# Kernel optimization log

Hardware: AMD Instinct MI355X
Metric: run time of the kernel (lower is better)

## Reference

```python
import jax, jax.numpy as jnp
import numpy as np


def cayley_batch(data):
    # data: (b, r, r). Q = (I + skew) @ (I - skew)^{-1}  (torch solve with left=False)
    b, rr, _ = data.shape
    skew = 0.5 * (data - data.transpose(0, 2, 1))
    I = jnp.eye(rr, dtype=data.dtype)
    A = I - skew  # always invertible (skew-symmetric)
    B = I + skew
    # Solve X @ A = B  ->  A^T X^T = B^T
    Q = jnp.linalg.solve(A.transpose(0, 2, 1), B.transpose(0, 2, 1)).transpose(0, 2, 1)
    return Q


def blockdiag_butterfly_multiply(x, w1, w2):
    # x: (batch, n); w1: (k, q, p) with k*p == n; w2: (l, s, r) with l*r == k*q
    batch = x.shape[0]
    k, q, p = w1.shape
    l, s, r = w2.shape
    out1 = jnp.einsum('bkp,kqp->bkq', x.reshape(batch, k, p), w1)  # (batch, k, q)
    # flat (k*q) viewed as (r, l), then transposed -> (batch, l, r)
    out1 = out1.reshape(batch, r, l).transpose(0, 2, 1)
    out2 = jnp.einsum('blr,lsr->bls', out1, w2)  # (batch, l, s)
    # permute to (batch, s, l) and flatten -> (batch, s*l)
    return out2.transpose(0, 2, 1).reshape(batch, s * l)


def setup_inputs() -> dict:
    key = jax.random.key(0)
    k1, k2, k3 = jax.random.split(key, 3)
    n, nblocks = 4096, 64
    bs = n // nblocks  # 64
    x = jax.random.normal(k1, (16384, n), dtype=jnp.float32)
    L = jax.random.normal(k2, (nblocks, bs, bs), dtype=jnp.float32)
    R = jax.random.normal(k3, (nblocks, bs, bs), dtype=jnp.float32)
    return {"x": x, "L": L, "R": R}


def reference(x, L, R):
    # GSOrthogonal.forward with orthogonal=True, method='cayley':
    # orthogonalize L and R, then butterfly multiply with (x, R_orth, L_orth)
    Lq = cayley_batch(L)
    Rq = cayley_batch(R)
    return blockdiag_butterfly_multiply(x, Rq, Lq)
```

## Files before the change

kernel.cpp:

```cpp
#include <hip/hip_runtime.h>
#include <hip/hip_bf16.h>

typedef __bf16 bf16x4 __attribute__((ext_vector_type(4)));
typedef __bf16 bf16x8 __attribute__((ext_vector_type(8)));
typedef float  floatx4 __attribute__((ext_vector_type(4)));

__global__ __launch_bounds__(256) void cayley_pack_kernel(
    const float* __restrict__ L, const float* __restrict__ R,
    __bf16* __restrict__ ws) {
  __shared__ float Ms[64][65];
  __shared__ float Pa[2][64];
  __shared__ float Pi[2][64];
  __shared__ float fcol[2][64];

  const int blk = blockIdx.x;
  const int t = threadIdx.x;
  const float* M = (blk < 64) ? (R + (size_t)blk * 4096)
                              : (L + (size_t)(blk - 64) * 4096);
  __bf16* dst = ws + (size_t)blk * 4096;

  for (int u = 0; u < 16; ++u) {
    int idx = u * 256 + t;
    Ms[idx >> 6][idx & 63] = M[idx];
  }
  __syncthreads();

  const int i = t >> 2;
  const int g = t & 3;
  const int jb = g * 16;
  float a[16], v[16];
#pragma unroll
  for (int jj = 0; jj < 16; ++jj) {
    int j = jb + jj;
    float s = 0.5f * (Ms[i][j] - Ms[j][i]);
    a[jj] = (i == j ? 1.0f : 0.0f) - s;
    v[jj] = (i == j ? 1.0f : 0.0f);
  }
  __syncthreads();

  for (int k = 0; k < 64; ++k) {
    const int kb = k & 1;
    if (g == (k >> 4)) fcol[kb][i] = a[k & 15];
    if (i == k) {
#pragma unroll
      for (int jj = 0; jj < 16; ++jj) { Pa[kb][jb + jj] = a[jj]; Pi[kb][jb + jj] = v[jj]; }
    }
    __syncthreads();
    const float ip = 1.0f / Pa[kb][k];
    if (i == k) {
#pragma unroll
      for (int jj = 0; jj < 16; ++jj) { a[jj] *= ip; v[jj] *= ip; }
    } else {
      const float f = fcol[kb][i] * ip;
#pragma unroll
      for (int jj = 0; jj < 16; ++jj) {
        a[jj] -= f * Pa[kb][jb + jj];
        v[jj] -= f * Pi[kb][jb + jj];
      }
    }
  }

#pragma unroll
  for (int jj = 0; jj < 16; ++jj) {
    int j = jb + jj;
    Ms[i][j] = 2.0f * v[jj] - (i == j ? 1.0f : 0.0f);
  }
  __syncthreads();

  const int lane = t & 63;
  const int grp = t >> 6;
  const int colq = lane & 15;
  const int quad = lane >> 4;
#pragma unroll
  for (int kh = 0; kh < 2; ++kh) {
    bf16x8 pk;
#pragma unroll
    for (int j8 = 0; j8 < 8; ++j8)
      pk[j8] = (__bf16)Ms[16 * grp + colq][32 * kh + 8 * quad + j8];
    *(bf16x8*)(dst + (kh * 4 + grp) * 512 + lane * 8) = pk;
  }
}

__global__ __launch_bounds__(512, 2) void butterfly_kernel(
    const float* __restrict__ x, const __bf16* __restrict__ ws,
    float* __restrict__ out) {
  extern __shared__ short interS[];
  __bf16* inter = (__bf16*)interS;
  float* bounce = (float*)interS;

  const int t = threadIdx.x;
  const int wv = t >> 6;
  const int lane = t & 63;
  const int col = lane & 15;
  const int quad = lane >> 4;
  const size_t b0 = (size_t)blockIdx.x * 16;

  const __bf16* w1 = ws;
  const __bf16* w2 = ws + 64 * 4096;

  const float* xrow = x + (b0 + (size_t)col) * 4096;
#pragma unroll
  for (int rg = 0; rg < 2; ++rg) {
    const int r0 = wv * 8 + rg * 4;
    floatx4 xu[4][2], xw[4][2];
#pragma unroll
    for (int ir = 0; ir < 4; ++ir) {
      const float* src = xrow + (r0 + ir) * 64 + quad * 8;
#pragma unroll
      for (int kh = 0; kh < 2; ++kh) {
        xu[ir][kh] = *(const floatx4*)(src + kh * 32);
        xw[ir][kh] = *(const floatx4*)(src + kh * 32 + 4);
      }
    }
    bf16x8 wfr[2][4][2];
#pragma unroll
    for (int ir = 0; ir < 4; ++ir)
#pragma unroll
      for (int kh = 0; kh < 2; ++kh)
        wfr[0][ir][kh] = *(const bf16x8*)(
            w1 + (size_t)(r0 + ir) * 4096 + (kh * 4 + 0) * 512 + lane * 8);
    bf16x8 af[4][2];
#pragma unroll
    for (int ir = 0; ir < 4; ++ir)
#pragma unroll
      for (int kh = 0; kh < 2; ++kh) {
        bf16x8 f;
        f[0] = (__bf16)xu[ir][kh][0]; f[1] = (__bf16)xu[ir][kh][1];
        f[2] = (__bf16)xu[ir][kh][2]; f[3] = (__bf16)xu[ir][kh][3];
        f[4] = (__bf16)xw[ir][kh][0]; f[5] = (__bf16)xw[ir][kh][1];
        f[6] = (__bf16)xw[ir][kh][2]; f[7] = (__bf16)xw[ir][kh][3];
        af[ir][kh] = f;
      }
#pragma unroll
    for (int qc = 0; qc < 4; ++qc) {
      if (qc < 3) {
#pragma unroll
        for (int ir = 0; ir < 4; ++ir)
#pragma unroll
          for (int kh = 0; kh < 2; ++kh)
            wfr[(qc + 1) & 1][ir][kh] = *(const bf16x8*)(
                w1 + (size_t)(r0 + ir) * 4096 + (kh * 4 + qc + 1) * 512 + lane * 8);
      }
      floatx4 vals[4];
#pragma unroll
      for (int ir = 0; ir < 4; ++ir) {
        floatx4 acc = {0.f, 0.f, 0.f, 0.f};
        acc = __builtin_amdgcn_mfma_f32_16x16x32_bf16(af[ir][0], wfr[qc & 1][ir][0], acc, 0, 0, 0);
        acc = __builtin_amdgcn_mfma_f32_16x16x32_bf16(af[ir][1], wfr[qc & 1][ir][1], acc, 0, 0, 0);
        vals[ir] = acc;
      }
      const int l = qc * 16 + col;
#pragma unroll
      for (int reg = 0; reg < 4; ++reg) {
        const int b = quad * 4 + reg;
        bf16x4 pk;
        pk[0] = (__bf16)vals[0][reg];
        pk[1] = (__bf16)vals[1][reg];
        pk[2] = (__bf16)vals[2][reg];
        pk[3] = (__bf16)vals[3][reg];
        const int cs = wv ^ (b & 7) ^ (l & 7);
        *(bf16x4*)(inter + l * 1024 + b * 64 + cs * 8 + rg * 4) = pk;
      }
    }
  }
  __syncthreads();

  bf16x8 A0[8], A1[8];
#pragma unroll
  for (int l16 = 0; l16 < 8; ++l16) {
    const int l = wv * 8 + l16;
    const int swz = (col & 7) ^ (l & 7);
    A0[l16] = *(const bf16x8*)(inter + l * 1024 + col * 64 + (quad ^ swz) * 8);
    A1[l16] = *(const bf16x8*)(inter + l * 1024 + col * 64 + ((4 + quad) ^ swz) * 8);
  }
  __syncthreads();

  float* outb = out + b0 * 4096;
#pragma unroll
  for (int p = 0; p < 2; ++p) {
    bf16x8 wf2[2][2][2];
#pragma unroll
    for (int scloc = 0; scloc < 2; ++scloc)
#pragma unroll
      for (int kh = 0; kh < 2; ++kh)
        wf2[0][scloc][kh] = *(const bf16x8*)(
            w2 + (size_t)(wv * 8) * 4096 + (kh * 4 + p * 2 + scloc) * 512 + lane * 8);
    floatx4 acc[8][2];
#pragma unroll
    for (int l16 = 0; l16 < 8; ++l16) {
      if (l16 < 7) {
        const int ln = wv * 8 + l16 + 1;
#pragma unroll
        for (int scloc = 0; scloc < 2; ++scloc)
#pragma unroll
          for (int kh = 0; kh < 2; ++kh)
            wf2[(l16 + 1) & 1][scloc][kh] = *(const bf16x8*)(
                w2 + (size_t)ln * 4096 + (kh * 4 + p * 2 + scloc) * 512 + lane * 8);
      }
#pragma unroll
      for (int scloc = 0; scloc < 2; ++scloc) {
        floatx4 a = {0.f, 0.f, 0.f, 0.f};
        a = __builtin_amdgcn_mfma_f32_16x16x32_bf16(A0[l16], wf2[l16 & 1][scloc][0], a, 0, 0, 0);
        a = __builtin_amdgcn_mfma_f32_16x16x32_bf16(A1[l16], wf2[l16 & 1][scloc][1], a, 0, 0, 0);
        acc[l16][scloc] = a;
      }
    }
#pragma unroll
    for (int scloc = 0; scloc < 2; ++scloc)
#pragma unroll
      for (int reg = 0; reg < 4; ++reg)
#pragma unroll
        for (int h = 0; h < 2; ++h) {
          const int b = quad * 4 + reg;
          const int g = b * 512 + scloc * 256 + col * 16 + wv * 2 + h;
          const int gp = g ^ ((g >> 4) & 7);
          floatx4 pk;
          pk[0] = acc[h * 4 + 0][scloc][reg];
          pk[1] = acc[h * 4 + 1][scloc][reg];
          pk[2] = acc[h * 4 + 2][scloc][reg];
          pk[3] = acc[h * 4 + 3][scloc][reg];
          *(floatx4*)(bounce + gp * 4) = pk;
        }
    __syncthreads();
#pragma unroll
    for (int rr = 0; rr < 2; ++rr) {
      const int b = wv * 2 + rr;
#pragma unroll
      for (int i = 0; i < 8; ++i) {
        const int g = b * 512 + i * 64 + lane;
        const int gp = g ^ ((g >> 4) & 7);
        floatx4 v = *(const floatx4*)(bounce + gp * 4);
        *(floatx4*)(outb + (size_t)b * 4096 + p * 2048 + i * 256 + lane * 4) = v;
      }
    }
    __syncthreads();
  }
}

extern "C" void kernel_launch(void* const* d_in, const int* in_sizes, int n_in,
                              void* d_out, int out_size, void* d_ws, size_t ws_size,
                              hipStream_t stream) {
  const float* x = (const float*)d_in[0];
  const float* L = (const float*)d_in[1];
  const float* R = (const float*)d_in[2];
  float* out = (float*)d_out;
  __bf16* ws = (__bf16*)d_ws;

  const int nrows = in_sizes[0] / 4096;

  cayley_pack_kernel<<<128, 256, 0, stream>>>(L, R, ws);
  butterfly_kernel<<<nrows / 16, 512, 131072, stream>>>(x, ws, out);
}
```

Measured before the change: 522.2 us.

## Software-pipeline x/w1 loads and compute all stage-2 outputs in one pass

Stage 1 is restructured so the second row group's x loads and the w1 fragments are issued ahead of the MFMAs that consume them, overlapping global loads with compute. Stage 2 now computes all four output column chunks in a single pass over l, streaming A fragments from LDS with double buffering instead of preloading all of them. This removes one pass of w2 reloads and keeps 32 accumulators live, which raises register pressure and may hurt the launch bound of 2 blocks per SM. It also adds partial unrolling of the Cayley elimination loop.

```diff
diff --git a/kernel.cpp b/kernel.cpp
--- a/kernel.cpp
+++ b/kernel.cpp
@@ -38,6 +38,7 @@
   }
   __syncthreads();
 
+#pragma unroll 2
   for (int k = 0; k < 64; ++k) {
     const int kb = k & 1;
     if (g == (k >> 4)) fcol[kb][i] = a[k & 15];
@@ -99,27 +100,19 @@
   const __bf16* w2 = ws + 64 * 4096;
 
   const float* xrow = x + (b0 + (size_t)col) * 4096;
-#pragma unroll
-  for (int rg = 0; rg < 2; ++rg) {
-    const int r0 = wv * 8 + rg * 4;
-    floatx4 xu[4][2], xw[4][2];
+
+  auto loadX = [&](int r0loc, floatx4 (&xu)[4][2], floatx4 (&xw)[4][2]) {
 #pragma unroll
     for (int ir = 0; ir < 4; ++ir) {
-      const float* src = xrow + (r0 + ir) * 64 + quad * 8;
+      const float* src = xrow + (r0loc + ir) * 64 + quad * 8;
 #pragma unroll
       for (int kh = 0; kh < 2; ++kh) {
         xu[ir][kh] = *(const floatx4*)(src + kh * 32);
         xw[ir][kh] = *(const floatx4*)(src + kh * 32 + 4);
       }
     }
-    bf16x8 wfr[2][4][2];
-#pragma unroll
-    for (int ir = 0; ir < 4; ++ir)
-#pragma unroll
-      for (int kh = 0; kh < 2; ++kh)
-        wfr[0][ir][kh] = *(const bf16x8*)(
-            w1 + (size_t)(r0 + ir) * 4096 + (kh * 4 + 0) * 512 + lane * 8);
-    bf16x8 af[4][2];
+  };
+  auto cvtX = [&](floatx4 (&xu)[4][2], floatx4 (&xw)[4][2], bf16x8 (&af)[4][2]) {
 #pragma unroll
     for (int ir = 0; ir < 4; ++ir)
 #pragma unroll
@@ -131,80 +124,109 @@
         f[6] = (__bf16)xw[ir][kh][2]; f[7] = (__bf16)xw[ir][kh][3];
         af[ir][kh] = f;
       }
-#pragma unroll
-    for (int qc = 0; qc < 4; ++qc) {
-      if (qc < 3) {
-#pragma unroll
-        for (int ir = 0; ir < 4; ++ir)
-#pragma unroll
-          for (int kh = 0; kh < 2; ++kh)
-            wfr[(qc + 1) & 1][ir][kh] = *(const bf16x8*)(
-                w1 + (size_t)(r0 + ir) * 4096 + (kh * 4 + qc + 1) * 512 + lane * 8);
-      }
-      floatx4 vals[4];
-#pragma unroll
-      for (int ir = 0; ir < 4; ++ir) {
-        floatx4 acc = {0.f, 0.f, 0.f, 0.f};
-        acc = __builtin_amdgcn_mfma_f32_16x16x32_bf16(af[ir][0], wfr[qc & 1][ir][0], acc, 0, 0, 0);
-        acc = __builtin_amdgcn_mfma_f32_16x16x32_bf16(af[ir][1], wfr[qc & 1][ir][1], acc, 0, 0, 0);
-        vals[ir] = acc;
-      }
-      const int l = qc * 16 + col;
-#pragma unroll
-      for (int reg = 0; reg < 4; ++reg) {
-        const int b = quad * 4 + reg;
-        bf16x4 pk;
-        pk[0] = (__bf16)vals[0][reg];
-        pk[1] = (__bf16)vals[1][reg];
-        pk[2] = (__bf16)vals[2][reg];
-        pk[3] = (__bf16)vals[3][reg];
-        const int cs = wv ^ (b & 7) ^ (l & 7);
-        *(bf16x4*)(inter + l * 1024 + b * 64 + cs * 8 + rg * 4) = pk;
-      }
-    }
-  }
-  __syncthreads();
-
-  bf16x8 A0[8], A1[8];
-#pragma unroll
-  for (int l16 = 0; l16 < 8; ++l16) {
-    const int l = wv * 8 + l16;
+  };
+  auto loadW1 = [&](int r0loc, int qc, bf16x8 (&wf)[4][2]) {
+#pragma unroll
+    for (int ir = 0; ir < 4; ++ir)
+#pragma unroll
+      for (int kh = 0; kh < 2; ++kh)
+        wf[ir][kh] = *(const bf16x8*)(
+            w1 + (size_t)(r0loc + ir) * 4096 + (kh * 4 + qc) * 512 + lane * 8);
+  };
+  auto doQC = [&](int rg, int qc, bf16x8 (&af)[4][2], bf16x8 (&wf)[4][2]) {
+    floatx4 vals[4];
+#pragma unroll
+    for (int ir = 0; ir < 4; ++ir) {
+      floatx4 acc = {0.f, 0.f, 0.f, 0.f};
+      acc = __builtin_amdgcn_mfma_f32_16x16x32_bf16(af[ir][0], wf[ir][0], acc, 0, 0, 0);
+      acc = __builtin_amdgcn_mfma_f32_16x16x32_bf16(af[ir][1], wf[ir][1], acc, 0, 0, 0);
+      vals[ir] = acc;
+    }
+    const int l = qc * 16 + col;
+#pragma unroll
+    for (int reg = 0; reg < 4; ++reg) {
+      const int b = quad * 4 + reg;
+      bf16x4 pk;
+      pk[0] = (__bf16)vals[0][reg];
+      pk[1] = (__bf16)vals[1][reg];
+      pk[2] = (__bf16)vals[2][reg];
+      pk[3] = (__bf16)vals[3][reg];
+      const int cs = wv ^ (b & 7) ^ (l & 7);
+      *(bf16x4*)(inter + l * 1024 + b * 64 + cs * 8 + rg * 4) = pk;
+    }
+  };
+
+  {
+    const int rA = wv * 8;
+    const int rB = wv * 8 + 4;
+    floatx4 xu0[4][2], xw0[4][2];
+    loadX(rA, xu0, xw0);
+    bf16x8 wf[4][4][2];
+    loadW1(rA, 0, wf[0]);
+    loadW1(rA, 1, wf[1]);
+    bf16x8 af0[4][2];
+    cvtX(xu0, xw0, af0);
+    floatx4 xu1[4][2], xw1[4][2];
+    loadX(rB, xu1, xw1);
+    loadW1(rA, 2, wf[2]);
+    doQC(0, 0, af0, wf[0]);
+    loadW1(rA, 3, wf[3]);
+    doQC(0, 1, af0, wf[1]);
+    loadW1(rB, 0, wf[0]);
+    doQC(0, 2, af0, wf[2]);
+    loadW1(rB, 1, wf[1]);
+    doQC(0, 3, af0, wf[3]);
+    bf16x8 af1[4][2];
+    cvtX(xu1, xw1, af1);
+    loadW1(rB, 2, wf[2]);
+    doQC(1, 0, af1, wf[0]);
+    loadW1(rB, 3, wf[3]);
+    doQC(1, 1, af1, wf[1]);
+    doQC(1, 2, af1, wf[2]);
+    doQC(1, 3, af1, wf[3]);
+  }
+  __syncthreads();
+
+  auto loadA = [&](int l, bf16x8& a0, bf16x8& a1) {
     const int swz = (col & 7) ^ (l & 7);
-    A0[l16] = *(const bf16x8*)(inter + l * 1024 + col * 64 + (quad ^ swz) * 8);
-    A1[l16] = *(const bf16x8*)(inter + l * 1024 + col * 64 + ((4 + quad) ^ swz) * 8);
-  }
-  __syncthreads();
-
-  float* outb = out + b0 * 4096;
-#pragma unroll
-  for (int p = 0; p < 2; ++p) {
-    bf16x8 wf2[2][2][2];
-#pragma unroll
-    for (int scloc = 0; scloc < 2; ++scloc)
+    a0 = *(const bf16x8*)(inter + l * 1024 + col * 64 + (quad ^ swz) * 8);
+    a1 = *(const bf16x8*)(inter + l * 1024 + col * 64 + ((4 + quad) ^ swz) * 8);
+  };
+  auto loadW2 = [&](int l, bf16x8 (&wf)[4][2]) {
+#pragma unroll
+    for (int sc = 0; sc < 4; ++sc)
 #pragma unroll
       for (int kh = 0; kh < 2; ++kh)
-        wf2[0][scloc][kh] = *(const bf16x8*)(
-            w2 + (size_t)(wv * 8) * 4096 + (kh * 4 + p * 2 + scloc) * 512 + lane * 8);
-    floatx4 acc[8][2];
+        wf[sc][kh] = *(const bf16x8*)(
+            w2 + (size_t)l * 4096 + (kh * 4 + sc) * 512 + lane * 8);
+  };
+
+  floatx4 acc[8][4];
+  {
+    bf16x8 A0[2], A1[2];
+    bf16x8 w2f[2][4][2];
+    loadA(wv * 8, A0[0], A1[0]);
+    loadW2(wv * 8, w2f[0]);
 #pragma unroll
     for (int l16 = 0; l16 < 8; ++l16) {
       if (l16 < 7) {
-        const int ln = wv * 8 + l16 + 1;
-#pragma unroll
-        for (int scloc = 0; scloc < 2; ++scloc)
-#pragma unroll
-          for (int kh = 0; kh < 2; ++kh)
-            wf2[(l16 + 1) & 1][scloc][kh] = *(const bf16x8*)(
-                w2 + (size_t)ln * 4096 + (kh * 4 + p * 2 + scloc) * 512 + lane * 8);
-      }
-#pragma unroll
-      for (int scloc = 0; scloc < 2; ++scloc) {
+        loadA(wv * 8 + l16 + 1, A0[(l16 + 1) & 1], A1[(l16 + 1) & 1]);
+        loadW2(wv * 8 + l16 + 1, w2f[(l16 + 1) & 1]);
+      }
+#pragma unroll
+      for (int sc = 0; sc < 4; ++sc) {
         floatx4 a = {0.f, 0.f, 0.f, 0.f};
-        a = __builtin_amdgcn_mfma_f32_16x16x32_bf16(A0[l16], wf2[l16 & 1][scloc][0], a, 0, 0, 0);
-        a = __builtin_amdgcn_mfma_f32_16x16x32_bf16(A1[l16], wf2[l16 & 1][scloc][1], a, 0, 0, 0);
-        acc[l16][scloc] = a;
-      }
-    }
+        a = __builtin_amdgcn_mfma_f32_16x16x32_bf16(A0[l16 & 1], w2f[l16 & 1][sc][0], a, 0, 0, 0);
+        a = __builtin_amdgcn_mfma_f32_16x16x32_bf16(A1[l16 & 1], w2f[l16 & 1][sc][1], a, 0, 0, 0);
+        acc[l16][sc] = a;
+      }
+    }
+  }
+  __syncthreads();
+
+  float* outb = out + b0 * 4096;
+#pragma unroll
+  for (int p = 0; p < 2; ++p) {
 #pragma unroll
     for (int scloc = 0; scloc < 2; ++scloc)
 #pragma unroll
@@ -215,10 +237,10 @@
           const int g = b * 512 + scloc * 256 + col * 16 + wv * 2 + h;
           const int gp = g ^ ((g >> 4) & 7);
           floatx4 pk;
-          pk[0] = acc[h * 4 + 0][scloc][reg];
-          pk[1] = acc[h * 4 + 1][scloc][reg];
-          pk[2] = acc[h * 4 + 2][scloc][reg];
-          pk[3] = acc[h * 4 + 3][scloc][reg];
+          pk[0] = acc[h * 4 + 0][p * 2 + scloc][reg];
+          pk[1] = acc[h * 4 + 1][p * 2 + scloc][reg];
+          pk[2] = acc[h * 4 + 2][p * 2 + scloc][reg];
+          pk[3] = acc[h * 4 + 3][p * 2 + scloc][reg];
           *(floatx4*)(bounce + gp * 4) = pk;
         }
     __syncthreads();
```

Result: faster. 505.2 us (-3.3%).
